# Performance work log

Hardware: AMD Instinct MI355X
Metric: run time of the kernel (lower is better)

Reference implementation:

```python
import jax, jax.numpy as jnp
import numpy as np

NUM_HEADS = 16


def setup_inputs() -> dict:
    key = jax.random.key(0)
    k1, k2, k3 = jax.random.split(key, 3)
    B, S, D = 2, 2048, 1024
    x = jax.random.normal(k1, (B, S, D), dtype=jnp.float32)
    # qkv_bias=False -> no bias on qkv projection; output Dense has default bias
    w_qkv = jax.random.normal(k2, (D, 3 * D), dtype=jnp.float32) * (1.0 / np.sqrt(D))
    w_out = jax.random.normal(k3, (D, D), dtype=jnp.float32) * (1.0 / np.sqrt(D))
    b_out = jnp.zeros((D,), dtype=jnp.float32)
    return {"x": x, "w_qkv": w_qkv, "w_out": w_out, "b_out": b_out}


def reference(x, w_qkv, w_out, b_out):
    B, S, D = x.shape
    H = NUM_HEADS
    Dh = D // H
    scale = 1.0 / np.sqrt(Dh).astype(np.float32)

    qkv = jnp.einsum('bsd,de->bse', x, w_qkv)           # [B,S,3D]
    q, k, v = jnp.split(qkv, 3, axis=-1)
    split = lambda t: t.reshape(B, S, H, Dh).transpose(0, 2, 1, 3)  # [B,H,S,Dh]
    q, k, v = split(q), split(k), split(v)

    attn = jnp.einsum('bhid,bhjd->bhij', q, k) * scale  # [B,H,S,S]
    # mask=None -> all-ones mask combined with causal mask => causal float mask
    causal = jnp.tril(jnp.ones((S, S), dtype=jnp.float32))[None, None]
    attn = causal * attn + (1.0 - causal) * (-1e9)
    attn = jax.nn.softmax(attn, axis=-1)

    out = jnp.einsum('bhij,bhjd->bhid', attn, v)        # [B,H,S,Dh]
    out = out.transpose(0, 2, 1, 3).reshape(B, S, D)    # merge heads
    return jnp.einsum('bsd,de->bse', out, w_out) + b_out
```

## Files before the change

### kernel.cpp

```cpp
#include <hip/hip_runtime.h>

typedef unsigned short u16;
typedef __bf16 bf16x8 __attribute__((ext_vector_type(8)));
typedef unsigned short u16x8 __attribute__((ext_vector_type(8)));
typedef float f32x4 __attribute__((ext_vector_type(4)));

union Frag { u16x8 u; bf16x8 b; };

__device__ __forceinline__ u16 f2bf(float f) {
  unsigned u = __builtin_bit_cast(unsigned, f);
  u += 0x7fff + ((u >> 16) & 1);
  return (u16)(u >> 16);
}

__device__ __forceinline__ f32x4 mfma16(bf16x8 a, bf16x8 b, f32x4 c) {
  return __builtin_amdgcn_mfma_f32_16x16x32_bf16(a, b, c, 0, 0, 0);
}

__device__ __forceinline__ float exp2_raw(float x) {
  float r;
  asm("v_exp_f32 %0, %1" : "=v"(r) : "v"(x));
  return r;
}

typedef const __attribute__((address_space(1))) void* as1cv;
typedef __attribute__((address_space(3))) void* as3v;

__device__ __forceinline__ void glds16(const u16* g, u16* l) {
  __builtin_amdgcn_global_load_lds((as1cv)g, (as3v)l, 16, 0, 0);
}

__global__ __launch_bounds__(256) void castf_bf(const float* __restrict__ src,
                                                u16* __restrict__ dst, int n4) {
  int i = blockIdx.x * blockDim.x + threadIdx.x;
  int stride = gridDim.x * blockDim.x;
  for (; i < n4; i += stride) {
    float4 v = ((const float4*)src)[i];
    ushort4 o;
    o.x = f2bf(v.x); o.y = f2bf(v.y); o.z = f2bf(v.z); o.w = f2bf(v.w);
    ((ushort4*)dst)[i] = o;
  }
}

__global__ __launch_bounds__(256) void cast_transpose2(const float* __restrict__ s1,
                                                       u16* __restrict__ d1,
                                                       const float* __restrict__ s2,
                                                       u16* __restrict__ d2) {
  __shared__ float tile[32][33];
  int bid = blockIdx.x;
  const float* src; u16* dst; int N;
  if (bid < 3072) { src = s1; dst = d1; N = 3072; }
  else            { bid -= 3072; src = s2; dst = d2; N = 1024; }
  const int K = 1024;
  int tn = N >> 5;
  int bk = bid / tn, bn = bid % tn;
  int k0 = bk << 5, n0 = bn << 5;
  int tx = threadIdx.x, ty = threadIdx.y;
#pragma unroll
  for (int i = 0; i < 4; i++)
    tile[ty + 8 * i][tx] = src[(size_t)(k0 + ty + 8 * i) * N + n0 + tx];
  __syncthreads();
#pragma unroll
  for (int i = 0; i < 4; i++)
    dst[(size_t)(n0 + ty + 8 * i) * K + k0 + tx] = f2bf(tile[tx][ty + 8 * i]);
}

__global__ __launch_bounds__(256) void gemm_qkv(const u16* __restrict__ A,
                                                const u16* __restrict__ BT,
                                                u16* __restrict__ C,
                                                u16* __restrict__ vt,
                                                int N, int K, int nbc) {
  __shared__ u16 Al[2][128 * 32];
  __shared__ u16 Bl[2][128 * 32];
  int nwg = gridDim.x;
  int bid = blockIdx.x;
  int swz = (bid & 7) * (nwg >> 3) + (bid >> 3);
  int br = swz / nbc, bc = swz % nbc;
  int tid = threadIdx.x;
  int w = tid >> 6, l = tid & 63;
  int lg = l >> 4, lq = l & 15;
  int wr = w >> 1, wc = w & 1;

  f32x4 acc[4][4];
#pragma unroll
  for (int m = 0; m < 4; m++)
#pragma unroll
    for (int n = 0; n < 4; n++)
      acc[m][n] = (f32x4){0.f, 0.f, 0.f, 0.f};

  const u16* Ab = A + (size_t)(br * 128 + 32 * w + (l >> 2)) * K + (l & 3) * 8;
  const u16* Bb = BT + (size_t)(bc * 128 + 32 * w + (l >> 2)) * K + (l & 3) * 8;

  auto stage = [&](int it, int buf) {
    int kt = it * 32;
    u16* ald = &Al[buf][32 * w * 32];
    u16* bld = &Bl[buf][32 * w * 32];
    glds16(Ab + kt, ald);
    glds16(Ab + (size_t)16 * K + kt, ald + 16 * 32);
    glds16(Bb + kt, bld);
    glds16(Bb + (size_t)16 * K + kt, bld + 16 * 32);
  };

  int nk = K >> 5;
  stage(0, 0);
  __syncthreads();

  for (int it = 0; it < nk; ++it) {
    int buf = it & 1;
    if (it + 1 < nk) stage(it + 1, buf ^ 1);

    Frag af[4], bf[4];
#pragma unroll
    for (int m = 0; m < 4; m++)
      af[m].u = *(const u16x8*)(&Al[buf][(64 * wr + 16 * m + lq) * 32 + lg * 8]);
#pragma unroll
    for (int n = 0; n < 4; n++)
      bf[n].u = *(const u16x8*)(&Bl[buf][(64 * wc + 16 * n + lq) * 32 + lg * 8]);
    __builtin_amdgcn_s_setprio(1);
#pragma unroll
    for (int m = 0; m < 4; m++)
#pragma unroll
      for (int n = 0; n < 4; n++)
        acc[m][n] = mfma16(af[m].b, bf[n].b, acc[m][n]);
    __builtin_amdgcn_s_setprio(0);
    __syncthreads();
  }

  int row0 = br * 128 + 64 * wr + lg * 4;
  int col0 = bc * 128 + 64 * wc + lq;
  if (bc < 16) {
#pragma unroll
    for (int n = 0; n < 4; n++)
#pragma unroll
      for (int m = 0; m < 4; m++)
#pragma unroll
        for (int r = 0; r < 4; r++)
          C[(size_t)(row0 + 16 * m + r) * N + col0 + 16 * n] = f2bf(acc[m][n][r]);
  } else {
#pragma unroll
    for (int n = 0; n < 4; n++) {
      int vcol = col0 + 16 * n - 2048;
      int h = vcol >> 6, dh = vcol & 63;
#pragma unroll
      for (int m = 0; m < 4; m++) {
        int s_abs = row0 + 16 * m;
        int bb = s_abs >> 11;
        int s = s_abs & 2047;
        int e = (s >> 5) * 32 + ((s >> 4) & 1) * 4 + ((s >> 2) & 3) * 8;
        ushort4 v;
        v.x = f2bf(acc[m][n][0]); v.y = f2bf(acc[m][n][1]);
        v.z = f2bf(acc[m][n][2]); v.w = f2bf(acc[m][n][3]);
        *(ushort4*)&vt[((size_t)(bb * 16 + h) * 64 + dh) * 2048 + e] = v;
      }
    }
  }
}

__global__ __launch_bounds__(256) void gemm_bt(const u16* __restrict__ A,
                                               const u16* __restrict__ BT,
                                               float* __restrict__ Cout,
                                               const float* __restrict__ bias,
                                               int N, int K, int nbc) {
  __shared__ u16 Al[2][128 * 32];
  __shared__ u16 Bl[2][128 * 32];
  int nwg = gridDim.x;
  int bid = blockIdx.x;
  int swz = (bid & 7) * (nwg >> 3) + (bid >> 3);
  int br = swz / nbc, bc = swz % nbc;
  int tid = threadIdx.x;
  int w = tid >> 6, l = tid & 63;
  int lg = l >> 4, lq = l & 15;
  int wr = w >> 1, wc = w & 1;

  f32x4 acc[4][4];
#pragma unroll
  for (int m = 0; m < 4; m++)
#pragma unroll
    for (int n = 0; n < 4; n++)
      acc[m][n] = (f32x4){0.f, 0.f, 0.f, 0.f};

  const u16* Ab = A + (size_t)(br * 128 + 32 * w + (l >> 2)) * K + (l & 3) * 8;
  const u16* Bb = BT + (size_t)(bc * 128 + 32 * w + (l >> 2)) * K + (l & 3) * 8;

  auto stage = [&](int it, int buf) {
    int kt = it * 32;
    u16* ald = &Al[buf][32 * w * 32];
    u16* bld = &Bl[buf][32 * w * 32];
    glds16(Ab + kt, ald);
    glds16(Ab + (size_t)16 * K + kt, ald + 16 * 32);
    glds16(Bb + kt, bld);
    glds16(Bb + (size_t)16 * K + kt, bld + 16 * 32);
  };

  int nk = K >> 5;
  stage(0, 0);
  __syncthreads();

  for (int it = 0; it < nk; ++it) {
    int buf = it & 1;
    if (it + 1 < nk) stage(it + 1, buf ^ 1);

    Frag af[4], bf[4];
#pragma unroll
    for (int m = 0; m < 4; m++)
      af[m].u = *(const u16x8*)(&Al[buf][(64 * wr + 16 * m + lq) * 32 + lg * 8]);
#pragma unroll
    for (int n = 0; n < 4; n++)
      bf[n].u = *(const u16x8*)(&Bl[buf][(64 * wc + 16 * n + lq) * 32 + lg * 8]);
    __builtin_amdgcn_s_setprio(1);
#pragma unroll
    for (int m = 0; m < 4; m++)
#pragma unroll
      for (int n = 0; n < 4; n++)
        acc[m][n] = mfma16(af[m].b, bf[n].b, acc[m][n]);
    __builtin_amdgcn_s_setprio(0);
    __syncthreads();
  }

  int row0 = br * 128 + 64 * wr + lg * 4;
  int col0 = bc * 128 + 64 * wc + lq;
#pragma unroll
  for (int n = 0; n < 4; n++) {
    float bv = bias[col0 + 16 * n];
#pragma unroll
    for (int m = 0; m < 4; m++)
#pragma unroll
      for (int r = 0; r < 4; r++)
        Cout[(size_t)(row0 + 16 * m + r) * N + col0 + 16 * n] = acc[m][n][r] + bv;
  }
}

__global__ __launch_bounds__(256) void flash_attn(const u16* __restrict__ qkv,
                                                  const u16* __restrict__ vt,
                                                  u16* __restrict__ aout) {
  __shared__ __align__(16) u16 pool[2][8192];
  const float SL2E = 0.18033688011112043f;
  int bid = blockIdx.x;
  int bh = bid & 31;
  int qb = 31 - (bid >> 5);
  int b = bh >> 4, h = bh & 15;
  int tid = threadIdx.x;
  int w = tid >> 6, l = tid & 63;
  int lg = l >> 4, lq = l & 15;
  int q0w = qb * 64 + w * 16;
  int qidx = q0w + lq;
  int ntiles = qb + 1;

  const size_t rs = 3072;
  int srw = l >> 3;
  int scol = 8 * ((l & 7) ^ srw);
  const u16* kg = qkv + (size_t)(b * 2048) * rs + 1024 + h * 64;
  const u16* vg = vt + (size_t)bh * 64 * 2048;
  int r0 = (w * 2 + 0) * 8 + srw;
  int r1 = (w * 2 + 1) * 8 + srw;
  int swz = (lq & 7) << 3;

  Frag qf0, qf1;
  const u16* qbase = qkv + (size_t)(b * 2048 + q0w + lq) * rs + h * 64 + lg * 8;
  qf0.u = *(const u16x8*)(qbase);
  qf1.u = *(const u16x8*)(qbase + 32);

  float lam = 0.f;
  f32x4 o[4];
#pragma unroll
  for (int d = 0; d < 4; ++d) o[d] = (f32x4){0.f, 0.f, 0.f, 0.f};

  auto stage = [&](int tile, int buf) {
    int kt2 = tile * 64;
    u16* nb = &pool[buf][0];
    glds16(kg + (size_t)(kt2 + r0) * rs + scol, nb + (w * 2 + 0) * 512);
    glds16(kg + (size_t)(kt2 + r1) * rs + scol, nb + (w * 2 + 1) * 512);
    glds16(vg + (size_t)r0 * 2048 + kt2 + scol, nb + 4096 + (w * 2 + 0) * 512);
    glds16(vg + (size_t)r1 * 2048 + kt2 + scol, nb + 4096 + (w * 2 + 1) * 512);
  };

  stage(0, 0);
  __syncthreads();

  for (int t = 0; t < ntiles; ++t) {
    if (t + 1 < ntiles) stage(t + 1, (t + 1) & 1);
    const u16* Kl = &pool[t & 1][0];
    const u16* Vl = &pool[t & 1][4096];
    int kt = t * 64;

    f32x4 s[4];
    __builtin_amdgcn_s_setprio(1);
#pragma unroll
    for (int sub = 0; sub < 4; ++sub) {
      int row = sub * 16 + lq;
      Frag k0, k1;
      k0.u = *(const u16x8*)(Kl + row * 64 + ((lg * 8) ^ swz));
      k1.u = *(const u16x8*)(Kl + row * 64 + ((32 + lg * 8) ^ swz));
      f32x4 z = {0.f, 0.f, 0.f, 0.f};
      s[sub] = mfma16(k0.b, qf0.b, z);
      s[sub] = mfma16(k1.b, qf1.b, s[sub]);
    }
    __builtin_amdgcn_s_setprio(0);

    if (t == qb) {
#pragma unroll
      for (int sub = 0; sub < 4; ++sub)
#pragma unroll
        for (int r = 0; r < 4; ++r) {
          int key = kt + sub * 16 + lg * 4 + r;
          if (key > qidx) s[sub][r] = -1e30f;
        }
    }

    Frag pf[2];
#pragma unroll
    for (int hf = 0; hf < 2; ++hf)
#pragma unroll
      for (int r = 0; r < 4; ++r) {
        float p0 = exp2_raw(s[2 * hf][r] * SL2E);
        float p1 = exp2_raw(s[2 * hf + 1][r] * SL2E);
        lam += p0 + p1;
        pf[hf].b[r] = (__bf16)p0;
        pf[hf].b[4 + r] = (__bf16)p1;
      }

    __builtin_amdgcn_s_setprio(1);
#pragma unroll
    for (int d = 0; d < 4; ++d) {
      int row = d * 16 + lq;
      Frag vf0, vf1;
      vf0.u = *(const u16x8*)(Vl + row * 64 + ((lg * 8) ^ swz));
      vf1.u = *(const u16x8*)(Vl + row * 64 + ((32 + lg * 8) ^ swz));
      o[d] = mfma16(vf0.b, pf[0].b, o[d]);
      o[d] = mfma16(vf1.b, pf[1].b, o[d]);
    }
    __builtin_amdgcn_s_setprio(0);
    __syncthreads();
  }

  lam += __shfl_xor(lam, 16);
  lam += __shfl_xor(lam, 32);
  float inv = 1.0f / lam;

  u16* Ost = &pool[0][0] + w * (16 * 72);
#pragma unroll
  for (int d = 0; d < 4; ++d)
#pragma unroll
    for (int r = 0; r < 4; ++r)
      Ost[lq * 72 + d * 16 + lg * 4 + r] = f2bf(o[d][r] * inv);
  int q = l >> 2, c16 = (l & 3) * 16;
  u16x8 t0, t1;
#pragma unroll
  for (int j = 0; j < 8; j++) { t0[j] = Ost[q * 72 + c16 + j]; t1[j] = Ost[q * 72 + c16 + 8 + j]; }
  u16* orow = aout + (size_t)(b * 2048 + qb * 64 + w * 16 + q) * 1024 + h * 64 + c16;
  *(u16x8*)orow = t0;
  *(u16x8*)(orow + 8) = t1;
}

extern "C" void kernel_launch(void* const* d_in, const int* in_sizes, int n_in,
                              void* d_out, int out_size, void* d_ws, size_t ws_size,
                              hipStream_t stream) {
  const float* x    = (const float*)d_in[0];
  const float* wqkv = (const float*)d_in[1];
  const float* wout = (const float*)d_in[2];
  const float* bout = (const float*)d_in[3];
  float* out = (float*)d_out;

  char* ws = (char*)d_ws;
  u16* xb    = (u16*)(ws);
  u16* wqkvT = (u16*)(ws + 8388608);
  u16* woutT = (u16*)(ws + 14680064);
  u16* qkvb  = (u16*)(ws + 16777216);
  u16* vtb   = (u16*)(ws + 41943040);
  u16* aoutb = (u16*)(ws + 50331648);

  castf_bf<<<1024, 256, 0, stream>>>(x, xb, (4096 * 1024) / 4);
  cast_transpose2<<<3072 + 1024, dim3(32, 8), 0, stream>>>(wqkv, wqkvT, wout, woutT);

  gemm_qkv<<<(4096 / 128) * (3072 / 128), 256, 0, stream>>>(xb, wqkvT, qkvb, vtb,
                                                            3072, 1024, 3072 / 128);
  flash_attn<<<1024, 256, 0, stream>>>(qkvb, vtb, aoutb);

  gemm_bt<<<(4096 / 128) * (1024 / 128), 256, 0, stream>>>(aoutb, woutT, out, bout,
                                                           1024, 1024, 1024 / 128);
}
```

Measured before the change: 106.0 us.

## Process two query blocks per attention workgroup and merge cast kernels

Each flash-attention workgroup now handles 128 queries (two 64-row blocks) and shares every staged K/V tile between both, which halves K/V global loads and the grid size. Workgroups are ordered so early and late blocks pair up to balance causal work. Separately, the x cast and the weight cast-transposes are merged into one launch to save a kernel launch. The cost is roughly double the accumulator registers per wave, which may lower occupancy, and only 512 workgroups are launched.

```diff
diff --git a/kernel.cpp b/kernel.cpp
--- a/kernel.cpp
+++ b/kernel.cpp
@@ -30,32 +30,36 @@
   __builtin_amdgcn_global_load_lds((as1cv)g, (as3v)l, 16, 0, 0);
 }
 
-__global__ __launch_bounds__(256) void castf_bf(const float* __restrict__ src,
-                                                u16* __restrict__ dst, int n4) {
-  int i = blockIdx.x * blockDim.x + threadIdx.x;
-  int stride = gridDim.x * blockDim.x;
-  for (; i < n4; i += stride) {
-    float4 v = ((const float4*)src)[i];
-    ushort4 o;
-    o.x = f2bf(v.x); o.y = f2bf(v.y); o.z = f2bf(v.z); o.w = f2bf(v.w);
-    ((ushort4*)dst)[i] = o;
-  }
-}
-
-__global__ __launch_bounds__(256) void cast_transpose2(const float* __restrict__ s1,
-                                                       u16* __restrict__ d1,
-                                                       const float* __restrict__ s2,
-                                                       u16* __restrict__ d2) {
+__global__ __launch_bounds__(256) void prep(const float* __restrict__ x,
+                                            u16* __restrict__ xb,
+                                            const float* __restrict__ wqkv,
+                                            u16* __restrict__ wqkvT,
+                                            const float* __restrict__ wout,
+                                            u16* __restrict__ woutT) {
   __shared__ float tile[32][33];
   int bid = blockIdx.x;
+  int tid = threadIdx.x;
+  if (bid >= 4096) {
+    int i = (bid - 4096) * 256 + tid;
+    const int stride = 1024 * 256;
+#pragma unroll
+    for (int k = 0; k < 4; ++k) {
+      float4 v = ((const float4*)x)[i];
+      ushort4 o;
+      o.x = f2bf(v.x); o.y = f2bf(v.y); o.z = f2bf(v.z); o.w = f2bf(v.w);
+      ((ushort4*)xb)[i] = o;
+      i += stride;
+    }
+    return;
+  }
   const float* src; u16* dst; int N;
-  if (bid < 3072) { src = s1; dst = d1; N = 3072; }
-  else            { bid -= 3072; src = s2; dst = d2; N = 1024; }
+  if (bid < 3072) { src = wqkv; dst = wqkvT; N = 3072; }
+  else            { bid -= 3072; src = wout; dst = woutT; N = 1024; }
   const int K = 1024;
   int tn = N >> 5;
   int bk = bid / tn, bn = bid % tn;
   int k0 = bk << 5, n0 = bn << 5;
-  int tx = threadIdx.x, ty = threadIdx.y;
+  int tx = tid & 31, ty = tid >> 5;
 #pragma unroll
   for (int i = 0; i < 4; i++)
     tile[ty + 8 * i][tx] = src[(size_t)(k0 + ty + 8 * i) * N + n0 + tx];
@@ -237,14 +241,16 @@
   const float SL2E = 0.18033688011112043f;
   int bid = blockIdx.x;
   int bh = bid & 31;
-  int qb = 31 - (bid >> 5);
+  int g = bid >> 5;
+  int qb = (g < 8) ? (15 - g) : (g - 8);
   int b = bh >> 4, h = bh & 15;
   int tid = threadIdx.x;
   int w = tid >> 6, l = tid & 63;
   int lg = l >> 4, lq = l & 15;
-  int q0w = qb * 64 + w * 16;
-  int qidx = q0w + lq;
-  int ntiles = qb + 1;
+  int qA = qb * 128 + w * 16 + lq;
+  int qB = qA + 64;
+  int lastA = 2 * qb;
+  int ntiles = 2 * qb + 2;
 
   const size_t rs = 3072;
   int srw = l >> 3;
@@ -255,15 +261,20 @@
   int r1 = (w * 2 + 1) * 8 + srw;
   int swz = (lq & 7) << 3;
 
-  Frag qf0, qf1;
-  const u16* qbase = qkv + (size_t)(b * 2048 + q0w + lq) * rs + h * 64 + lg * 8;
-  qf0.u = *(const u16x8*)(qbase);
-  qf1.u = *(const u16x8*)(qbase + 32);
-
-  float lam = 0.f;
-  f32x4 o[4];
-#pragma unroll
-  for (int d = 0; d < 4; ++d) o[d] = (f32x4){0.f, 0.f, 0.f, 0.f};
+  const u16* qbase = qkv + (size_t)(b * 2048 + qb * 128 + w * 16 + lq) * rs + h * 64 + lg * 8;
+  Frag qA0, qA1, qB0, qB1;
+  qA0.u = *(const u16x8*)(qbase);
+  qA1.u = *(const u16x8*)(qbase + 32);
+  qB0.u = *(const u16x8*)(qbase + 64 * rs);
+  qB1.u = *(const u16x8*)(qbase + 64 * rs + 32);
+
+  f32x4 lam4A = {0.f, 0.f, 0.f, 0.f}, lam4B = {0.f, 0.f, 0.f, 0.f};
+  f32x4 oA[4], oB[4];
+#pragma unroll
+  for (int d = 0; d < 4; ++d) {
+    oA[d] = (f32x4){0.f, 0.f, 0.f, 0.f};
+    oB[d] = (f32x4){0.f, 0.f, 0.f, 0.f};
+  }
 
   auto stage = [&](int tile, int buf) {
     int kt2 = tile * 64;
@@ -282,8 +293,9 @@
     const u16* Kl = &pool[t & 1][0];
     const u16* Vl = &pool[t & 1][4096];
     int kt = t * 64;
-
-    f32x4 s[4];
+    bool doA = (t <= lastA);
+
+    f32x4 sA[4], sB[4];
     __builtin_amdgcn_s_setprio(1);
 #pragma unroll
     for (int sub = 0; sub < 4; ++sub) {
@@ -292,31 +304,56 @@
       k0.u = *(const u16x8*)(Kl + row * 64 + ((lg * 8) ^ swz));
       k1.u = *(const u16x8*)(Kl + row * 64 + ((32 + lg * 8) ^ swz));
       f32x4 z = {0.f, 0.f, 0.f, 0.f};
-      s[sub] = mfma16(k0.b, qf0.b, z);
-      s[sub] = mfma16(k1.b, qf1.b, s[sub]);
+      if (doA) {
+        sA[sub] = mfma16(k0.b, qA0.b, z);
+        sA[sub] = mfma16(k1.b, qA1.b, sA[sub]);
+      }
+      sB[sub] = mfma16(k0.b, qB0.b, z);
+      sB[sub] = mfma16(k1.b, qB1.b, sB[sub]);
     }
     __builtin_amdgcn_s_setprio(0);
 
-    if (t == qb) {
+    if (t == lastA) {
 #pragma unroll
       for (int sub = 0; sub < 4; ++sub)
 #pragma unroll
         for (int r = 0; r < 4; ++r) {
           int key = kt + sub * 16 + lg * 4 + r;
-          if (key > qidx) s[sub][r] = -1e30f;
+          if (key > qA) sA[sub][r] = -1e30f;
         }
     }
-
-    Frag pf[2];
+    if (t == lastA + 1) {
+#pragma unroll
+      for (int sub = 0; sub < 4; ++sub)
+#pragma unroll
+        for (int r = 0; r < 4; ++r) {
+          int key = kt + sub * 16 + lg * 4 + r;
+          if (key > qB) sB[sub][r] = -1e30f;
+        }
+    }
+
+    Frag pfA[2], pfB[2];
+    if (doA) {
+#pragma unroll
+      for (int hf = 0; hf < 2; ++hf)
+#pragma unroll
+        for (int r = 0; r < 4; ++r) {
+          float p0 = exp2_raw(sA[2 * hf][r] * SL2E);
+          float p1 = exp2_raw(sA[2 * hf + 1][r] * SL2E);
+          lam4A[r] += p0 + p1;
+          pfA[hf].b[r] = (__bf16)p0;
+          pfA[hf].b[4 + r] = (__bf16)p1;
+        }
+    }
 #pragma unroll
     for (int hf = 0; hf < 2; ++hf)
 #pragma unroll
       for (int r = 0; r < 4; ++r) {
-        float p0 = exp2_raw(s[2 * hf][r] * SL2E);
-        float p1 = exp2_raw(s[2 * hf + 1][r] * SL2E);
-        lam += p0 + p1;
-        pf[hf].b[r] = (__bf16)p0;
-        pf[hf].b[4 + r] = (__bf16)p1;
+        float p0 = exp2_raw(sB[2 * hf][r] * SL2E);
+        float p1 = exp2_raw(sB[2 * hf + 1][r] * SL2E);
+        lam4B[r] += p0 + p1;
+        pfB[hf].b[r] = (__bf16)p0;
+        pfB[hf].b[4 + r] = (__bf16)p1;
       }
 
     __builtin_amdgcn_s_setprio(1);
@@ -326,30 +363,56 @@
       Frag vf0, vf1;
       vf0.u = *(const u16x8*)(Vl + row * 64 + ((lg * 8) ^ swz));
       vf1.u = *(const u16x8*)(Vl + row * 64 + ((32 + lg * 8) ^ swz));
-      o[d] = mfma16(vf0.b, pf[0].b, o[d]);
-      o[d] = mfma16(vf1.b, pf[1].b, o[d]);
+      if (doA) {
+        oA[d] = mfma16(vf0.b, pfA[0].b, oA[d]);
+        oA[d] = mfma16(vf1.b, pfA[1].b, oA[d]);
+      }
+      oB[d] = mfma16(vf0.b, pfB[0].b, oB[d]);
+      oB[d] = mfma16(vf1.b, pfB[1].b, oB[d]);
     }
     __builtin_amdgcn_s_setprio(0);
     __syncthreads();
   }
 
-  lam += __shfl_xor(lam, 16);
-  lam += __shfl_xor(lam, 32);
-  float inv = 1.0f / lam;
-
-  u16* Ost = &pool[0][0] + w * (16 * 72);
-#pragma unroll
-  for (int d = 0; d < 4; ++d)
-#pragma unroll
-    for (int r = 0; r < 4; ++r)
-      Ost[lq * 72 + d * 16 + lg * 4 + r] = f2bf(o[d][r] * inv);
+  float lamA = lam4A[0] + lam4A[1] + lam4A[2] + lam4A[3];
+  lamA += __shfl_xor(lamA, 16);
+  lamA += __shfl_xor(lamA, 32);
+  float lamB = lam4B[0] + lam4B[1] + lam4B[2] + lam4B[3];
+  lamB += __shfl_xor(lamB, 16);
+  lamB += __shfl_xor(lamB, 32);
+
   int q = l >> 2, c16 = (l & 3) * 16;
-  u16x8 t0, t1;
-#pragma unroll
-  for (int j = 0; j < 8; j++) { t0[j] = Ost[q * 72 + c16 + j]; t1[j] = Ost[q * 72 + c16 + 8 + j]; }
-  u16* orow = aout + (size_t)(b * 2048 + qb * 64 + w * 16 + q) * 1024 + h * 64 + c16;
-  *(u16x8*)orow = t0;
-  *(u16x8*)(orow + 8) = t1;
+  {
+    u16* Ost = &pool[0][0] + w * (16 * 72);
+    float inv = 1.0f / lamA;
+#pragma unroll
+    for (int d = 0; d < 4; ++d)
+#pragma unroll
+      for (int r = 0; r < 4; ++r)
+        Ost[lq * 72 + d * 16 + lg * 4 + r] = f2bf(oA[d][r] * inv);
+    u16x8 t0, t1;
+#pragma unroll
+    for (int j = 0; j < 8; j++) { t0[j] = Ost[q * 72 + c16 + j]; t1[j] = Ost[q * 72 + c16 + 8 + j]; }
+    u16* orow = aout + (size_t)(b * 2048 + qb * 128 + w * 16 + q) * 1024 + h * 64 + c16;
+    *(u16x8*)orow = t0;
+    *(u16x8*)(orow + 8) = t1;
+  }
+  __syncthreads();
+  {
+    u16* Ost = &pool[1][0] + w * (16 * 72);
+    float inv = 1.0f / lamB;
+#pragma unroll
+    for (int d = 0; d < 4; ++d)
+#pragma unroll
+      for (int r = 0; r < 4; ++r)
+        Ost[lq * 72 + d * 16 + lg * 4 + r] = f2bf(oB[d][r] * inv);
+    u16x8 t0, t1;
+#pragma unroll
+    for (int j = 0; j < 8; j++) { t0[j] = Ost[q * 72 + c16 + j]; t1[j] = Ost[q * 72 + c16 + 8 + j]; }
+    u16* orow = aout + (size_t)(b * 2048 + qb * 128 + 64 + w * 16 + q) * 1024 + h * 64 + c16;
+    *(u16x8*)orow = t0;
+    *(u16x8*)(orow + 8) = t1;
+  }
 }
 
 extern "C" void kernel_launch(void* const* d_in, const int* in_sizes, int n_in,
@@ -369,12 +432,11 @@
   u16* vtb   = (u16*)(ws + 41943040);
   u16* aoutb = (u16*)(ws + 50331648);
 
-  castf_bf<<<1024, 256, 0, stream>>>(x, xb, (4096 * 1024) / 4);
-  cast_transpose2<<<3072 + 1024, dim3(32, 8), 0, stream>>>(wqkv, wqkvT, wout, woutT);
+  prep<<<5120, 256, 0, stream>>>(x, xb, wqkv, wqkvT, wout, woutT);
 
   gemm_qkv<<<(4096 / 128) * (3072 / 128), 256, 0, stream>>>(xb, wqkvT, qkvb, vtb,
                                                             3072, 1024, 3072 / 128);
-  flash_attn<<<1024, 256, 0, stream>>>(qkvb, vtb, aoutb);
+  flash_attn<<<512, 256, 0, stream>>>(qkvb, vtb, aoutb);
 
   gemm_bt<<<(4096 / 128) * (1024 / 128), 256, 0, stream>>>(aoutb, woutT, out, bout,
                                                            1024, 1024, 1024 / 128);
```

Measured after the change: 120.8 us. 1.14x slower.
